# Kernel tuning notes

Measured on AMD Instinct MI355X. Metric: run time of the kernel, lower is better.

The kernel has to match this reference:

```python
import jax, jax.numpy as jnp
import numpy as np

N_NODES = 100000
N_EDGES = 1600000
IN_DIM, HID, OUT = 64, 128, 128
NUM_GRAPHS = 64
BN_EPS = 1e-5


def setup_inputs() -> dict:
    key = jax.random.key(0)
    ks = jax.random.split(key, 16)
    x = jax.random.normal(ks[0], (N_NODES, IN_DIM), dtype=jnp.float32)
    edge_index = jax.random.randint(ks[1], (2, N_EDGES), 0, N_NODES, dtype=jnp.int32)
    batch = jnp.sort(jax.random.randint(ks[2], (N_NODES,), 0, NUM_GRAPHS, dtype=jnp.int32))
    dims = [IN_DIM, HID, HID, OUT]
    inp = {"x": x, "edge_index": edge_index, "batch": batch}
    for i in range(3):
        din, dout = dims[i], dims[i + 1]
        s = 1.0 / np.sqrt(din)
        inp[f"Ws{i}"] = jax.random.uniform(ks[3 + 4 * i], (din, dout), jnp.float32, -s, s)
        inp[f"Wi{i}"] = jax.random.uniform(ks[4 + 4 * i], (din, dout), jnp.float32, -s, s)
        inp[f"Wo{i}"] = jax.random.uniform(ks[5 + 4 * i], (din, dout), jnp.float32, -s, s)
        inp[f"g{i}"] = jnp.ones((dout,), jnp.float32)
        inp[f"b{i}"] = jnp.zeros((dout,), jnp.float32)
    return inp


def _dgcn(x, src, dst, Ws, Wi, Wo, gamma, beta):
    # directed aggregation: in-edges (messages from src land on dst) and out-edges
    agg_in = jax.ops.segment_sum(x[src], dst, num_segments=N_NODES)   # [N, d]
    agg_out = jax.ops.segment_sum(x[dst], src, num_segments=N_NODES)  # [N, d]
    out = x @ Ws + agg_in @ Wi + agg_out @ Wo
    out = jax.nn.relu(out)
    # BatchNorm1d (training mode, biased variance, as in torch)
    mu = out.mean(axis=0)
    var = ((out - mu) ** 2).mean(axis=0)
    return gamma * (out - mu) * jax.lax.rsqrt(var + BN_EPS) + beta


def reference(x, edge_index, batch, Ws0, Wi0, Wo0, g0, b0, Ws1, Wi1, Wo1, g1, b1,
              Ws2, Wi2, Wo2, g2, b2):
    src, dst = edge_index[0], edge_index[1]
    h = _dgcn(x, src, dst, Ws0, Wi0, Wo0, g0, b0)
    h = _dgcn(h, src, dst, Ws1, Wi1, Wo1, g1, b1)
    h = _dgcn(h, src, dst, Ws2, Wi2, Wo2, g2, b2)
    # global mean pool over graphs (dropout is identity at inference)
    sums = jax.ops.segment_sum(h, batch, num_segments=NUM_GRAPHS)       # [G, OUT]
    cnts = jax.ops.segment_sum(jnp.ones((N_NODES,), h.dtype), batch, num_segments=NUM_GRAPHS)
    return sums / jnp.maximum(cnts, 1.0)[:, None]
```

## Files before the change

### kernel.cpp

```cpp
#include <hip/hip_runtime.h>

#define NN 100000
#define NE 1600000
#define NG 64
#define BN_EPS 1e-5f

#define TOT (2 * NN)

#define NB 196
#define KPB 1024
#define BDEPTH 64
#define BCAP 18432
#define P1B 512
#define EPB ((NE + P1B - 1) / P1B)

#define GG 1563
#define PB 1600

typedef __attribute__((ext_vector_type(8))) _Float16 f16x8;
typedef __attribute__((ext_vector_type(8))) unsigned short u16x8;
typedef __attribute__((ext_vector_type(4))) float f32x4;

__device__ __forceinline__ float h2f(unsigned short u) {
  _Float16 h; __builtin_memcpy(&h, &u, 2); return (float)h;
}
__device__ __forceinline__ unsigned short f2h(float f) {
  _Float16 h = (_Float16)f; unsigned short u; __builtin_memcpy(&u, &h, 2); return u;
}

__device__ __forceinline__ int lower_bound_dev(const int* a, int n, int key) {
  int lo = 0, hi = n;
  while (lo < hi) { int mid = (lo + hi) >> 1; if (a[mid] < key) lo = mid + 1; else hi = mid; }
  return lo;
}

__global__ __launch_bounds__(256) void k_p1(const int* __restrict__ src,
    const int* __restrict__ dst, int* __restrict__ gcur, unsigned int* __restrict__ pairs) {
  __shared__ unsigned int lbuf[NB][BDEPTH];
  __shared__ int lcnt[NB], lbase[NB];
  __shared__ int sc[256];
  int t = threadIdx.x;
  if (t < NB) lcnt[t] = 0;
  __syncthreads();
  int e0 = blockIdx.x * EPB;
  int e1 = min(e0 + EPB, NE);
  for (int e = e0 + t; e < e1; e += 256) {
    int s = src[e], d = dst[e];
    {
      int key = d;
      unsigned int val = ((unsigned int)(key & (KPB - 1)) << 17) | (unsigned int)s;
      int bk = key >> 10;
      int p = atomicAdd(&lcnt[bk], 1);
      if (p < BDEPTH) lbuf[bk][p] = val;
      else { int g = atomicAdd(&gcur[bk], 1); pairs[(size_t)bk * BCAP + g] = val; }
    }
    {
      int key = s + NN;
      unsigned int val = ((unsigned int)(key & (KPB - 1)) << 17) | (unsigned int)d;
      int bk = key >> 10;
      int p = atomicAdd(&lcnt[bk], 1);
      if (p < BDEPTH) lbuf[bk][p] = val;
      else { int g = atomicAdd(&gcur[bk], 1); pairs[(size_t)bk * BCAP + g] = val; }
    }
  }
  __syncthreads();
  if (t < NB) {
    int c = min(lcnt[t], BDEPTH);
    lcnt[t] = c;
    lbase[t] = atomicAdd(&gcur[t], c);
  }
  __syncthreads();
  sc[t] = (t < NB) ? lcnt[t] : 0;
  __syncthreads();
  for (int off = 1; off < 256; off <<= 1) {
    int x = (t >= off) ? sc[t - off] : 0;
    __syncthreads();
    sc[t] += x;
    __syncthreads();
  }
  int total = sc[NB - 1];
  for (int idx = t; idx < total; idx += 256) {
    int lo = 0, hi = NB - 1;
    while (lo < hi) { int mid = (lo + hi) >> 1; if (sc[mid] > idx) hi = mid; else lo = mid + 1; }
    int within = idx - ((lo == 0) ? 0 : sc[lo - 1]);
    pairs[(size_t)lo * BCAP + lbase[lo] + within] = lbuf[lo][within];
  }
}

__global__ void k_scanNB(const int* __restrict__ gcur, int* __restrict__ fbase) {
  __shared__ int sc[256];
  int t = threadIdx.x;
  sc[t] = (t < NB) ? gcur[t] : 0;
  __syncthreads();
  for (int off = 1; off < 256; off <<= 1) {
    int x = (t >= off) ? sc[t - off] : 0;
    __syncthreads();
    sc[t] += x;
    __syncthreads();
  }
  if (t < NB) fbase[t] = (t == 0) ? 0 : sc[t - 1];
  if (t == 0) fbase[NB] = sc[NB - 1];
}

__global__ __launch_bounds__(256) void k_p2(const unsigned int* __restrict__ pairs,
    const int* __restrict__ gcur, const int* __restrict__ fbase,
    int* __restrict__ offs, int* __restrict__ nbr) {
  int b = blockIdx.x;
  int n = gcur[b];
  int base = fbase[b];
  __shared__ int hist[KPB];
  __shared__ int sc[256];
  int t = threadIdx.x;
  #pragma unroll
  for (int j = 0; j < 4; ++j) hist[t * 4 + j] = 0;
  __syncthreads();
  const unsigned int* bp = pairs + (size_t)b * BCAP;
  for (int i = t; i < n; i += 256) atomicAdd(&hist[bp[i] >> 17], 1);
  __syncthreads();
  int v[4]; int tsum = 0;
  #pragma unroll
  for (int j = 0; j < 4; ++j) { v[j] = hist[t * 4 + j]; tsum += v[j]; }
  sc[t] = tsum;
  __syncthreads();
  for (int off = 1; off < 256; off <<= 1) {
    int x = (t >= off) ? sc[t - off] : 0;
    __syncthreads();
    sc[t] += x;
    __syncthreads();
  }
  int run = (t == 0) ? 0 : sc[t - 1];
  #pragma unroll
  for (int j = 0; j < 4; ++j) {
    int key = b * KPB + t * 4 + j;
    if (key < TOT) offs[key] = base + run;
    hist[t * 4 + j] = run;
    run += v[j];
  }
  if (b == NB - 1 && t == 0) offs[TOT] = base + n;
  __syncthreads();
  for (int i = t; i < n; i += 256) {
    unsigned int u = bp[i];
    int lk = (int)(u >> 17);
    int pos = atomicAdd(&hist[lk], 1);
    nbr[base + pos] = (int)(u & 0x1FFFFu);
  }
}

__global__ __launch_bounds__(256) void k_cvt_x(const float* __restrict__ x,
                                               unsigned short* __restrict__ xb) {
  size_t i = (size_t)blockIdx.x * 256 + threadIdx.x;
  if (i >= (size_t)NN * 16) return;
  float4 v = *(const float4*)(x + i * 4);
  ushort4 o;
  o.x = f2h(v.x); o.y = f2h(v.y); o.z = f2h(v.z); o.w = f2h(v.w);
  *(ushort4*)(xb + i * 4) = o;
}

struct WtArgs { const float* W[9]; };
__global__ __launch_bounds__(256) void k_wt(WtArgs a, unsigned short* __restrict__ wt,
                                            float* __restrict__ ssid) {
  int t = blockIdx.x * 256 + threadIdx.x;
  if (t >= 15360) {
    int u = t - 15360;
    if (u < 128) { ssid[u] = 1.f; ssid[128 + u] = 0.f; }
    return;
  }
  int p, rem, KS;
  if (t < 3072) { p = t >> 10; rem = t & 1023; KS = 2; }
  else { int u = t - 3072; p = 3 + (u >> 11); rem = u & 2047; KS = 4; }
  int ks = rem >> 9;
  int rem2 = rem & 511;
  int nt = rem2 >> 6;
  int lane = rem2 & 63;
  int L = p / 3, op = p - L * 3;
  int lbase = (L == 0) ? 0 : (24576 + (L - 1) * 49152);
  size_t dst = (size_t)lbase + (size_t)op * KS * 4096 + (size_t)(ks * 8 + nt) * 512 + lane * 8;
  const float* W = a.W[p];
  int krow = ks * 32 + (lane >> 4) * 8;
  int col = nt * 16 + (lane & 15);
  #pragma unroll
  for (int j = 0; j < 8; ++j)
    wt[dst + j] = f2h(W[(size_t)(krow + j) * 128 + col]);
}

template<int DIN>
__global__ __launch_bounds__(256) void k_gather(const unsigned short* __restrict__ xb,
    const float* __restrict__ ss, const int* __restrict__ offs, const int* __restrict__ nbr,
    unsigned short* __restrict__ aggi, unsigned short* __restrict__ aggo) {
  constexpr int GW = DIN / 8;
  constexpr int GPB = 256 / GW;
  int g = blockIdx.x * GPB + threadIdx.x / GW;
  if (g >= TOT) return;
  int c0 = (threadIdx.x % GW) * 8;
  int beg = offs[g], end = offs[g + 1];
  f16x8 acc;
  #pragma unroll
  for (int j = 0; j < 8; ++j) acc[j] = (_Float16)0.f;
  int k = beg;
  for (; k + 4 <= end; k += 4) {
    int n0 = nbr[k], n1 = nbr[k + 1], n2 = nbr[k + 2], n3 = nbr[k + 3];
    f16x8 v0 = *(const f16x8*)(xb + (size_t)n0 * DIN + c0);
    f16x8 v1 = *(const f16x8*)(xb + (size_t)n1 * DIN + c0);
    f16x8 v2 = *(const f16x8*)(xb + (size_t)n2 * DIN + c0);
    f16x8 v3 = *(const f16x8*)(xb + (size_t)n3 * DIN + c0);
    acc += (v0 + v1) + (v2 + v3);
  }
  for (; k < end; ++k) {
    f16x8 v = *(const f16x8*)(xb + (size_t)nbr[k] * DIN + c0);
    acc += v;
  }
  float cnt = (float)(end - beg);
  union { u16x8 v; unsigned short u[8]; } r;
  #pragma unroll
  for (int j = 0; j < 8; ++j)
    r.u[j] = f2h(fmaf((float)acc[j], ss[c0 + j], cnt * ss[128 + c0 + j]));
  unsigned short* o = (g < NN) ? (aggi + (size_t)g * DIN) : (aggo + (size_t)(g - NN) * DIN);
  __builtin_nontemporal_store(r.v, (u16x8*)(o + c0));
}

template<int KD>
__global__ __launch_bounds__(256) void k_gemm(const unsigned short* __restrict__ A0,
    const float* __restrict__ ss, const unsigned short* __restrict__ A1,
    const unsigned short* __restrict__ A2, const unsigned short* __restrict__ wt,
    unsigned short* __restrict__ out, float* __restrict__ part) {
  constexpr int KS = KD / 32;
  int tid = threadIdx.x;
  int lane = tid & 63;
  int w = tid >> 6;
  int m0 = blockIdx.x * 64 + w * 16;
  int arow = m0 + (lane & 15);
  int koff = (lane >> 4) * 8;
  f32x4 acc[8];
  #pragma unroll
  for (int nt = 0; nt < 8; ++nt) acc[nt] = (f32x4){0.f, 0.f, 0.f, 0.f};

  const unsigned short* As[3] = {A0, A1, A2};
  #pragma unroll
  for (int op = 0; op < 3; ++op) {
    const unsigned short* __restrict__ A = As[op];
    f16x8 af[KS];
    if (arow < NN) {
      #pragma unroll
      for (int ks = 0; ks < KS; ++ks)
        af[ks] = *(const f16x8*)(A + (size_t)arow * KD + ks * 32 + koff);
      if (op == 0) {
        #pragma unroll
        for (int ks = 0; ks < KS; ++ks) {
          #pragma unroll
          for (int j = 0; j < 8; ++j) {
            int c = ks * 32 + koff + j;
            af[ks][j] = (_Float16)fmaf((float)af[ks][j], ss[c], ss[128 + c]);
          }
        }
      }
    } else {
      #pragma unroll
      for (int ks = 0; ks < KS; ++ks)
        #pragma unroll
        for (int j = 0; j < 8; ++j) af[ks][j] = (_Float16)0.f;
    }
    #pragma unroll
    for (int ks = 0; ks < KS; ++ks) {
      #pragma unroll
      for (int nt = 0; nt < 8; ++nt) {
        f16x8 bf = *(const f16x8*)(wt + ((size_t)(op * KS + ks) * 8 + nt) * 512 + lane * 8);
        acc[nt] = __builtin_amdgcn_mfma_f32_16x16x32_f16(af[ks], bf, acc[nt], 0, 0, 0);
      }
    }
  }

  __shared__ unsigned short lds[4][16][128];
  __shared__ float sws[4][128], sws2[4][128];
  float s8[8], s28[8];
  #pragma unroll
  for (int nt = 0; nt < 8; ++nt) { s8[nt] = 0.f; s28[nt] = 0.f; }
  #pragma unroll
  for (int nt = 0; nt < 8; ++nt)
    #pragma unroll
    for (int r = 0; r < 4; ++r) {
      float v = fmaxf(acc[nt][r], 0.f);
      lds[w][(lane >> 4) * 4 + r][nt * 16 + (lane & 15)] = f2h(v);
      s8[nt] += v;
      s28[nt] = fmaf(v, v, s28[nt]);
    }
  #pragma unroll
  for (int it = 0; it < 4; ++it) {
    int rr = (lane >> 4) + it * 4;
    int cc = (lane & 15) * 8;
    int grow = m0 + rr;
    if (grow < NN)
      *(u16x8*)(out + (size_t)grow * 128 + cc) = *(const u16x8*)&lds[w][rr][cc];
  }
  #pragma unroll
  for (int nt = 0; nt < 8; ++nt) {
    s8[nt]  += __shfl_xor(s8[nt], 16);
    s8[nt]  += __shfl_xor(s8[nt], 32);
    s28[nt] += __shfl_xor(s28[nt], 16);
    s28[nt] += __shfl_xor(s28[nt], 32);
  }
  if (lane < 16) {
    #pragma unroll
    for (int nt = 0; nt < 8; ++nt) {
      sws[w][nt * 16 + lane]  = s8[nt];
      sws2[w][nt * 16 + lane] = s28[nt];
    }
  }
  __syncthreads();
  if (tid < 128) {
    float S  = sws[0][tid] + sws[1][tid] + sws[2][tid] + sws[3][tid];
    float S2 = sws2[0][tid] + sws2[1][tid] + sws2[2][tid] + sws2[3][tid];
    part[(size_t)tid * PB + blockIdx.x]         = S;
    part[(size_t)(128 + tid) * PB + blockIdx.x] = S2;
  }
}

__global__ __launch_bounds__(256) void k_bn_final(const float* __restrict__ part,
    const float* __restrict__ g, const float* __restrict__ b, float* __restrict__ ss) {
  int c = blockIdx.x;
  int t = threadIdx.x;
  float s = 0.f, s2 = 0.f;
  for (int i = t; i < GG; i += 256) {
    s  += part[(size_t)c * PB + i];
    s2 += part[(size_t)(128 + c) * PB + i];
  }
  __shared__ float rs[256], rs2[256];
  rs[t] = s; rs2[t] = s2; __syncthreads();
  for (int off = 128; off > 0; off >>= 1) {
    if (t < off) { rs[t] += rs[t + off]; rs2[t] += rs2[t + off]; }
    __syncthreads();
  }
  if (t == 0) {
    float mu = rs[0] / (float)NN;
    float var = rs2[0] / (float)NN - mu * mu;
    float rcp = rsqrtf(var + BN_EPS);
    float sc = rcp * g[c];
    ss[c] = sc;
    ss[128 + c] = b[c] - mu * sc;
  }
}

__global__ __launch_bounds__(128) void k_pool(const unsigned short* __restrict__ hb,
    const int* __restrict__ batch, float* __restrict__ pool) {
  int c = threadIdx.x;
  int n0 = blockIdx.x * 256;
  if (n0 >= NN) return;
  int nend = n0 + 256; if (nend > NN) nend = NN;
  int cur = batch[n0];
  float run = 0.f;
  for (int n = n0; n < nend; ++n) {
    int g = batch[n];
    if (g != cur) { atomicAdd(&pool[(size_t)cur * 128 + c], run); run = 0.f; cur = g; }
    run += h2f(hb[(size_t)n * 128 + c]);
  }
  atomicAdd(&pool[(size_t)cur * 128 + c], run);
}

__global__ __launch_bounds__(128) void k_final(const float* __restrict__ pool,
    const int* __restrict__ batch, const float* __restrict__ ss, float* __restrict__ out) {
  int g = blockIdx.x;
  int c = threadIdx.x;
  __shared__ int cnt;
  if (c == 0) {
    int lo = lower_bound_dev(batch, NN, g);
    int hi = lower_bound_dev(batch, NN, g + 1);
    cnt = hi - lo;
  }
  __syncthreads();
  float d = (float)(cnt > 1 ? cnt : 1);
  out[(size_t)g * 128 + c] = fmaf(pool[(size_t)g * 128 + c] / d, ss[c], ss[128 + c]);
}

extern "C" void kernel_launch(void* const* d_in, const int* in_sizes, int n_in,
                              void* d_out, int out_size, void* d_ws, size_t ws_size,
                              hipStream_t stream) {
  const float* x     = (const float*)d_in[0];
  const int*   ei    = (const int*)d_in[1];
  const int*   batch = (const int*)d_in[2];
  const float* gg[3] = {(const float*)d_in[6], (const float*)d_in[11], (const float*)d_in[16]};
  const float* bbv[3]= {(const float*)d_in[7], (const float*)d_in[12], (const float*)d_in[17]};
  const int* src = ei;
  const int* dst = ei + NE;

  uintptr_t p = ((uintptr_t)d_ws + 255) & ~(uintptr_t)255;
  auto alloc = [&](size_t bytes) { uintptr_t r = p; p = (p + bytes + 255) & ~(uintptr_t)255; return r; };

  unsigned int* pairs = (unsigned int*)alloc((size_t)NB * BCAP * 4);
  int* gcur  = (int*)alloc(NB * 4);
  int* fbase = (int*)alloc((NB + 1) * 4);
  int* offs  = (int*)alloc((TOT + 1) * 4);
  int* nbr   = (int*)alloc((size_t)2 * NE * 4);
  unsigned short* xb   = (unsigned short*)alloc((size_t)NN * 64 * 2);
  unsigned short* hb0  = (unsigned short*)alloc((size_t)NN * 128 * 2);
  unsigned short* hb1  = (unsigned short*)alloc((size_t)NN * 128 * 2);
  unsigned short* hb2  = (unsigned short*)alloc((size_t)NN * 128 * 2);
  unsigned short* aggi = (unsigned short*)alloc((size_t)NN * 128 * 2);
  unsigned short* aggo = (unsigned short*)alloc((size_t)NN * 128 * 2);
  unsigned short* wt   = (unsigned short*)alloc(122880 * 2);
  float* part  = (float*)alloc((size_t)256 * PB * 4);
  float* ss_id = (float*)alloc(256 * 4);
  float* ss0   = (float*)alloc(256 * 4);
  float* ss1   = (float*)alloc(256 * 4);
  float* ss2   = (float*)alloc(256 * 4);
  float* pool  = (float*)alloc((size_t)NG * 128 * 4);

  hipMemsetAsync(gcur, 0, NB * sizeof(int), stream);
  k_p1<<<P1B, 256, 0, stream>>>(src, dst, gcur, pairs);
  k_scanNB<<<1, 256, 0, stream>>>(gcur, fbase);
  k_p2<<<NB, 256, 0, stream>>>(pairs, gcur, fbase, offs, nbr);

  k_cvt_x<<<(NN * 16 + 255) / 256, 256, 0, stream>>>(x, xb);
  WtArgs wa;
  wa.W[0] = (const float*)d_in[3];  wa.W[1] = (const float*)d_in[4];  wa.W[2] = (const float*)d_in[5];
  wa.W[3] = (const float*)d_in[8];  wa.W[4] = (const float*)d_in[9];  wa.W[5] = (const float*)d_in[10];
  wa.W[6] = (const float*)d_in[13]; wa.W[7] = (const float*)d_in[14]; wa.W[8] = (const float*)d_in[15];
  k_wt<<<61, 256, 0, stream>>>(wa, wt, ss_id);

  k_gather<64><<<(TOT + 31) / 32, 256, 0, stream>>>(xb, ss_id, offs, nbr, aggi, aggo);
  k_gemm<64><<<GG, 256, 0, stream>>>(xb, ss_id, aggi, aggo, wt + 0, hb0, part);
  k_bn_final<<<128, 256, 0, stream>>>(part, gg[0], bbv[0], ss0);

  k_gather<128><<<(TOT + 15) / 16, 256, 0, stream>>>(hb0, ss0, offs, nbr, aggi, aggo);
  k_gemm<128><<<GG, 256, 0, stream>>>(hb0, ss0, aggi, aggo, wt + 24576, hb1, part);
  k_bn_final<<<128, 256, 0, stream>>>(part, gg[1], bbv[1], ss1);

  k_gather<128><<<(TOT + 15) / 16, 256, 0, stream>>>(hb1, ss1, offs, nbr, aggi, aggo);
  k_gemm<128><<<GG, 256, 0, stream>>>(hb1, ss1, aggi, aggo, wt + 73728, hb2, part);
  k_bn_final<<<128, 256, 0, stream>>>(part, gg[2], bbv[2], ss2);

  hipMemsetAsync(pool, 0, (size_t)NG * 128 * 4, stream);
  k_pool<<<(NN + 255) / 256, 128, 0, stream>>>(hb2, batch, pool);
  k_final<<<NG, 128, 0, stream>>>(pool, batch, ss2, (float*)d_out);
}
```

Measured before the change: 567.1 us.

## Fuse neighbor gather-aggregation into the MFMA GEMM kernel per layer

Removes the separate gather kernel and its aggi/aggo intermediate buffers. Each GEMM thread now walks the CSR in- and out-neighbor lists for its own row, accumulating f16 sums in registers in the MFMA A-fragment layout before the three matmuls. This cuts the write and re-read of two N×D aggregate arrays and two launches per layer. In exchange, the gather parallelism drops: only 16 rows per wave, with each lane loading a 32-column strided slice. This gives less memory-level parallelism, more register pressure and poorer coalescing per neighbor row.

```diff
diff --git a/kernel.cpp b/kernel.cpp
--- a/kernel.cpp
+++ b/kernel.cpp
@@ -183,45 +183,10 @@
     wt[dst + j] = f2h(W[(size_t)(krow + j) * 128 + col]);
 }
 
-template<int DIN>
-__global__ __launch_bounds__(256) void k_gather(const unsigned short* __restrict__ xb,
+template<int KD>
+__global__ __launch_bounds__(256) void k_fgemm(const unsigned short* __restrict__ xb,
     const float* __restrict__ ss, const int* __restrict__ offs, const int* __restrict__ nbr,
-    unsigned short* __restrict__ aggi, unsigned short* __restrict__ aggo) {
-  constexpr int GW = DIN / 8;
-  constexpr int GPB = 256 / GW;
-  int g = blockIdx.x * GPB + threadIdx.x / GW;
-  if (g >= TOT) return;
-  int c0 = (threadIdx.x % GW) * 8;
-  int beg = offs[g], end = offs[g + 1];
-  f16x8 acc;
-  #pragma unroll
-  for (int j = 0; j < 8; ++j) acc[j] = (_Float16)0.f;
-  int k = beg;
-  for (; k + 4 <= end; k += 4) {
-    int n0 = nbr[k], n1 = nbr[k + 1], n2 = nbr[k + 2], n3 = nbr[k + 3];
-    f16x8 v0 = *(const f16x8*)(xb + (size_t)n0 * DIN + c0);
-    f16x8 v1 = *(const f16x8*)(xb + (size_t)n1 * DIN + c0);
-    f16x8 v2 = *(const f16x8*)(xb + (size_t)n2 * DIN + c0);
-    f16x8 v3 = *(const f16x8*)(xb + (size_t)n3 * DIN + c0);
-    acc += (v0 + v1) + (v2 + v3);
-  }
-  for (; k < end; ++k) {
-    f16x8 v = *(const f16x8*)(xb + (size_t)nbr[k] * DIN + c0);
-    acc += v;
-  }
-  float cnt = (float)(end - beg);
-  union { u16x8 v; unsigned short u[8]; } r;
-  #pragma unroll
-  for (int j = 0; j < 8; ++j)
-    r.u[j] = f2h(fmaf((float)acc[j], ss[c0 + j], cnt * ss[128 + c0 + j]));
-  unsigned short* o = (g < NN) ? (aggi + (size_t)g * DIN) : (aggo + (size_t)(g - NN) * DIN);
-  __builtin_nontemporal_store(r.v, (u16x8*)(o + c0));
-}
-
-template<int KD>
-__global__ __launch_bounds__(256) void k_gemm(const unsigned short* __restrict__ A0,
-    const float* __restrict__ ss, const unsigned short* __restrict__ A1,
-    const unsigned short* __restrict__ A2, const unsigned short* __restrict__ wt,
+    const unsigned short* __restrict__ wt,
     unsigned short* __restrict__ out, float* __restrict__ part) {
   constexpr int KS = KD / 32;
   int tid = threadIdx.x;
@@ -230,43 +195,121 @@
   int m0 = blockIdx.x * 64 + w * 16;
   int arow = m0 + (lane & 15);
   int koff = (lane >> 4) * 8;
-  f32x4 acc[8];
-  #pragma unroll
-  for (int nt = 0; nt < 8; ++nt) acc[nt] = (f32x4){0.f, 0.f, 0.f, 0.f};
-
-  const unsigned short* As[3] = {A0, A1, A2};
-  #pragma unroll
-  for (int op = 0; op < 3; ++op) {
-    const unsigned short* __restrict__ A = As[op];
-    f16x8 af[KS];
-    if (arow < NN) {
-      #pragma unroll
-      for (int ks = 0; ks < KS; ++ks)
-        af[ks] = *(const f16x8*)(A + (size_t)arow * KD + ks * 32 + koff);
-      if (op == 0) {
+  bool valid = arow < NN;
+
+  f16x8 a1[KS], a2[KS];
+  #pragma unroll
+  for (int ks = 0; ks < KS; ++ks) {
+    #pragma unroll
+    for (int j = 0; j < 8; ++j) { a1[ks][j] = (_Float16)0.f; a2[ks][j] = (_Float16)0.f; }
+  }
+  int cin = 0, cout = 0;
+  if (valid) {
+    {
+      int beg = offs[arow], end = offs[arow + 1];
+      cin = end - beg;
+      int k = beg;
+      for (; k + 2 <= end; k += 2) {
+        int n0 = nbr[k], n1 = nbr[k + 1];
+        const unsigned short* r0 = xb + (size_t)n0 * KD + koff;
+        const unsigned short* r1 = xb + (size_t)n1 * KD + koff;
         #pragma unroll
         for (int ks = 0; ks < KS; ++ks) {
-          #pragma unroll
-          for (int j = 0; j < 8; ++j) {
-            int c = ks * 32 + koff + j;
-            af[ks][j] = (_Float16)fmaf((float)af[ks][j], ss[c], ss[128 + c]);
-          }
+          f16x8 v0 = *(const f16x8*)(r0 + ks * 32);
+          f16x8 v1 = *(const f16x8*)(r1 + ks * 32);
+          a1[ks] += v0 + v1;
         }
       }
-    } else {
-      #pragma unroll
-      for (int ks = 0; ks < KS; ++ks)
+      if (k < end) {
+        const unsigned short* r0 = xb + (size_t)nbr[k] * KD + koff;
         #pragma unroll
-        for (int j = 0; j < 8; ++j) af[ks][j] = (_Float16)0.f;
-    }
+        for (int ks = 0; ks < KS; ++ks) a1[ks] += *(const f16x8*)(r0 + ks * 32);
+      }
+    }
+    {
+      int beg = offs[NN + arow], end = offs[NN + arow + 1];
+      cout = end - beg;
+      int k = beg;
+      for (; k + 2 <= end; k += 2) {
+        int n0 = nbr[k], n1 = nbr[k + 1];
+        const unsigned short* r0 = xb + (size_t)n0 * KD + koff;
+        const unsigned short* r1 = xb + (size_t)n1 * KD + koff;
+        #pragma unroll
+        for (int ks = 0; ks < KS; ++ks) {
+          f16x8 v0 = *(const f16x8*)(r0 + ks * 32);
+          f16x8 v1 = *(const f16x8*)(r1 + ks * 32);
+          a2[ks] += v0 + v1;
+        }
+      }
+      if (k < end) {
+        const unsigned short* r0 = xb + (size_t)nbr[k] * KD + koff;
+        #pragma unroll
+        for (int ks = 0; ks < KS; ++ks) a2[ks] += *(const f16x8*)(r0 + ks * 32);
+      }
+    }
+  }
+
+  f32x4 acc[8];
+  #pragma unroll
+  for (int nt = 0; nt < 8; ++nt) acc[nt] = (f32x4){0.f, 0.f, 0.f, 0.f};
+
+  f16x8 af[KS];
+  if (valid) {
     #pragma unroll
     for (int ks = 0; ks < KS; ++ks) {
+      f16x8 v = *(const f16x8*)(xb + (size_t)arow * KD + ks * 32 + koff);
+      #pragma unroll
+      for (int j = 0; j < 8; ++j) {
+        int c = ks * 32 + koff + j;
+        af[ks][j] = (_Float16)fmaf((float)v[j], ss[c], ss[128 + c]);
+      }
+    }
+  } else {
+    #pragma unroll
+    for (int ks = 0; ks < KS; ++ks)
+      #pragma unroll
+      for (int j = 0; j < 8; ++j) af[ks][j] = (_Float16)0.f;
+  }
+  #pragma unroll
+  for (int ks = 0; ks < KS; ++ks)
+    #pragma unroll
+    for (int nt = 0; nt < 8; ++nt) {
+      f16x8 bf = *(const f16x8*)(wt + ((size_t)(0 * KS + ks) * 8 + nt) * 512 + lane * 8);
+      acc[nt] = __builtin_amdgcn_mfma_f32_16x16x32_f16(af[ks], bf, acc[nt], 0, 0, 0);
+    }
+  {
+    float fc = (float)cin;
+    #pragma unroll
+    for (int ks = 0; ks < KS; ++ks)
+      #pragma unroll
+      for (int j = 0; j < 8; ++j) {
+        int c = ks * 32 + koff + j;
+        af[ks][j] = (_Float16)fmaf((float)a1[ks][j], ss[c], fc * ss[128 + c]);
+      }
+    #pragma unroll
+    for (int ks = 0; ks < KS; ++ks)
       #pragma unroll
       for (int nt = 0; nt < 8; ++nt) {
-        f16x8 bf = *(const f16x8*)(wt + ((size_t)(op * KS + ks) * 8 + nt) * 512 + lane * 8);
+        f16x8 bf = *(const f16x8*)(wt + ((size_t)(1 * KS + ks) * 8 + nt) * 512 + lane * 8);
         acc[nt] = __builtin_amdgcn_mfma_f32_16x16x32_f16(af[ks], bf, acc[nt], 0, 0, 0);
       }
-    }
+  }
+  {
+    float fc = (float)cout;
+    #pragma unroll
+    for (int ks = 0; ks < KS; ++ks)
+      #pragma unroll
+      for (int j = 0; j < 8; ++j) {
+        int c = ks * 32 + koff + j;
+        af[ks][j] = (_Float16)fmaf((float)a2[ks][j], ss[c], fc * ss[128 + c]);
+      }
+    #pragma unroll
+    for (int ks = 0; ks < KS; ++ks)
+      #pragma unroll
+      for (int nt = 0; nt < 8; ++nt) {
+        f16x8 bf = *(const f16x8*)(wt + ((size_t)(2 * KS + ks) * 8 + nt) * 512 + lane * 8);
+        acc[nt] = __builtin_amdgcn_mfma_f32_16x16x32_f16(af[ks], bf, acc[nt], 0, 0, 0);
+      }
   }
 
   __shared__ unsigned short lds[4][16][128];
@@ -393,8 +436,6 @@
   unsigned short* hb0  = (unsigned short*)alloc((size_t)NN * 128 * 2);
   unsigned short* hb1  = (unsigned short*)alloc((size_t)NN * 128 * 2);
   unsigned short* hb2  = (unsigned short*)alloc((size_t)NN * 128 * 2);
-  unsigned short* aggi = (unsigned short*)alloc((size_t)NN * 128 * 2);
-  unsigned short* aggo = (unsigned short*)alloc((size_t)NN * 128 * 2);
   unsigned short* wt   = (unsigned short*)alloc(122880 * 2);
   float* part  = (float*)alloc((size_t)256 * PB * 4);
   float* ss_id = (float*)alloc(256 * 4);
@@ -415,16 +456,13 @@
   wa.W[6] = (const float*)d_in[13]; wa.W[7] = (const float*)d_in[14]; wa.W[8] = (const float*)d_in[15];
   k_wt<<<61, 256, 0, stream>>>(wa, wt, ss_id);
 
-  k_gather<64><<<(TOT + 31) / 32, 256, 0, stream>>>(xb, ss_id, offs, nbr, aggi, aggo);
-  k_gemm<64><<<GG, 256, 0, stream>>>(xb, ss_id, aggi, aggo, wt + 0, hb0, part);
+  k_fgemm<64><<<GG, 256, 0, stream>>>(xb, ss_id, offs, nbr, wt + 0, hb0, part);
   k_bn_final<<<128, 256, 0, stream>>>(part, gg[0], bbv[0], ss0);
 
-  k_gather<128><<<(TOT + 15) / 16, 256, 0, stream>>>(hb0, ss0, offs, nbr, aggi, aggo);
-  k_gemm<128><<<GG, 256, 0, stream>>>(hb0, ss0, aggi, aggo, wt + 24576, hb1, part);
+  k_fgemm<128><<<GG, 256, 0, stream>>>(hb0, ss0, offs, nbr, wt + 24576, hb1, part);
   k_bn_final<<<128, 256, 0, stream>>>(part, gg[1], bbv[1], ss1);
 
-  k_gather<128><<<(TOT + 15) / 16, 256, 0, stream>>>(hb1, ss1, offs, nbr, aggi, aggo);
-  k_gemm<128><<<GG, 256, 0, stream>>>(hb1, ss1, aggi, aggo, wt + 73728, hb2, part);
+  k_fgemm<128><<<GG, 256, 0, stream>>>(hb1, ss1, offs, nbr, wt + 73728, hb2, part);
   k_bn_final<<<128, 256, 0, stream>>>(part, gg[2], bbv[2], ss2);
 
   hipMemsetAsync(pool, 0, (size_t)NG * 128 * 4, stream);
```

Result: slower. 630.8 us (+11.2%).
